# Optimization experiments

Hardware: AMD Instinct MI355X
Metric: run time of the kernel (lower is better)

## Reference

```python
import jax, jax.numpy as jnp
import numpy as np

# Production-scale dims (ENet decoder stage)
B, H, W, C = 8, 128, 128, 64
KH, KW = 2, 2  # kernel_size[1], kernel_size[2]
HOUT, WOUT = H * KH, W * KW


def setup_inputs() -> dict:
    key = jax.random.key(0)
    k1, k2, k3 = jax.random.split(key, 3)
    x = jax.random.normal(k1, (B, H, W, C), dtype=jnp.float32)
    # Build a valid max-pool argmax mask: each pooled cell picks one position
    # inside its KHxKW window; flat index = (h*WOUT + w)*C + c (TF argmax layout).
    dh = jax.random.randint(k2, (B, H, W, C), 0, KH)
    dw = jax.random.randint(k3, (B, H, W, C), 0, KW)
    h = jnp.arange(H)[:, None, None] * KH + dh   # [B,H,W,C]
    w = jnp.arange(W)[None, :, None] * KW + dw   # [B,H,W,C]
    c = jnp.arange(C)                            # [C]
    pool_mask = ((h * WOUT + w) * C + c).astype(jnp.int32)
    return {"input_pool": x, "pool_mask": pool_mask}


def reference(input_pool, pool_mask):
    # Faithful to tf.scatter_nd: decode flat per-batch indices and scatter
    # values into the zero-initialized upsampled output (duplicates add).
    b, h, w, c = input_pool.shape
    out_size = HOUT * WOUT * c
    flat_idx = pool_mask.reshape(b, -1)          # [B, H*W*C] indices into [HOUT*WOUT*C]
    vals = input_pool.reshape(b, -1)
    out = jnp.zeros((b, out_size), dtype=input_pool.dtype)
    out = out.at[jnp.arange(b)[:, None], flat_idx].add(vals)
    return out.reshape(b, HOUT, WOUT, c)
```

## Files before the change

### kernel.cpp

```cpp
#include <hip/hip_runtime.h>


#define Bsz   8
#define Hdim  128
#define Wdim  128
#define Cdim  64
#define HOUT  256
#define WOUT  256

__global__ __launch_bounds__(256) void maxunpool_gather(
    const float4* __restrict__ x,
    const int4*   __restrict__ mask,
    float4*       __restrict__ out)
{
    constexpr int CV = Cdim / 4;
    unsigned int tid = blockIdx.x * blockDim.x + threadIdx.x;

    int c4   = tid & (CV - 1);
    unsigned int r1 = tid >> 4;
    int wo   = r1 & (WOUT - 1);
    unsigned int r2 = r1 >> 8;
    int ho   = r2 & (HOUT - 1);
    int b    = r2 >> 8;

    int h = ho >> 1;
    int w = wo >> 1;

    unsigned int in_vec = ((unsigned int)(b * Hdim + h) * Wdim + w) * CV + c4;

    int4   m = mask[in_vec];
    float4 v = x[in_vec];

    int base = (ho * WOUT + wo) * Cdim + c4 * 4;

    float4 r;
    r.x = (m.x == base + 0) ? v.x : 0.0f;
    r.y = (m.y == base + 1) ? v.y : 0.0f;
    r.z = (m.z == base + 2) ? v.z : 0.0f;
    r.w = (m.w == base + 3) ? v.w : 0.0f;

    out[tid] = r;
}

extern "C" void kernel_launch(void* const* d_in, const int* in_sizes, int n_in,
                              void* d_out, int out_size, void* d_ws, size_t ws_size,
                              hipStream_t stream) {
    const float4* x    = (const float4*)d_in[0];
    const int4*   mask = (const int4*)d_in[1];
    float4*       out  = (float4*)d_out;

    const int n_vec = out_size / 4;
    const int block = 256;
    const int grid  = n_vec / block;

    maxunpool_gather<<<grid, block, 0, stream>>>(x, mask, out);
}
```

Before: 177.9 us.

## Invert unpool to one thread per input, writing 2x2 window with nontemporal ops

Switches from an output-indexed gather, which reloaded each mask and input vector four times, to an input-indexed form. Each thread loads its mask and value once and writes all four output positions of its 2x2 window. Loads and stores use nontemporal builtins to avoid polluting caches with streaming data. The trade-off is four strided stores per thread and a quarter as many threads.

```diff
diff --git a/kernel.cpp b/kernel.cpp
--- a/kernel.cpp
+++ b/kernel.cpp
@@ -1,57 +1,64 @@
 #include <hip/hip_runtime.h>
 
 
-#define Bsz   8
 #define Hdim  128
 #define Wdim  128
 #define Cdim  64
 #define HOUT  256
 #define WOUT  256
+#define CV    (Cdim / 4)
 
-__global__ __launch_bounds__(256) void maxunpool_gather(
-    const float4* __restrict__ x,
-    const int4*   __restrict__ mask,
-    float4*       __restrict__ out)
+typedef float vf4 __attribute__((ext_vector_type(4)));
+typedef int   vi4 __attribute__((ext_vector_type(4)));
+
+__global__ __launch_bounds__(256) void maxunpool_scatter(
+    const vf4* __restrict__ x,
+    const vi4* __restrict__ mask,
+    vf4*       __restrict__ out)
 {
-    constexpr int CV = Cdim / 4;
     unsigned int tid = blockIdx.x * blockDim.x + threadIdx.x;
 
-    int c4   = tid & (CV - 1);
-    unsigned int r1 = tid >> 4;
-    int wo   = r1 & (WOUT - 1);
-    unsigned int r2 = r1 >> 8;
-    int ho   = r2 & (HOUT - 1);
-    int b    = r2 >> 8;
+    int c4 = tid & (CV - 1);
+    unsigned int p = tid >> 4;
+    int w = p & (Wdim - 1);
+    unsigned int q = p >> 7;
+    int h = q & (Hdim - 1);
+    int b = q >> 7;
 
-    int h = ho >> 1;
-    int w = wo >> 1;
+    vi4 m = __builtin_nontemporal_load(&mask[tid]);
+    vf4 v = __builtin_nontemporal_load(&x[tid]);
 
-    unsigned int in_vec = ((unsigned int)(b * Hdim + h) * Wdim + w) * CV + c4;
+    int ho = h << 1;
+    int wo = w << 1;
 
-    int4   m = mask[in_vec];
-    float4 v = x[in_vec];
+    unsigned int o00 = ((unsigned int)(b * HOUT + ho) * WOUT + wo) * CV + c4;
 
-    int base = (ho * WOUT + wo) * Cdim + c4 * 4;
-
-    float4 r;
-    r.x = (m.x == base + 0) ? v.x : 0.0f;
-    r.y = (m.y == base + 1) ? v.y : 0.0f;
-    r.z = (m.z == base + 2) ? v.z : 0.0f;
-    r.w = (m.w == base + 3) ? v.w : 0.0f;
-
-    out[tid] = r;
+    #pragma unroll
+    for (int dh = 0; dh < 2; ++dh) {
+        #pragma unroll
+        for (int dw = 0; dw < 2; ++dw) {
+            int base = ((ho + dh) * WOUT + (wo + dw)) * Cdim + (c4 << 2);
+            vf4 r;
+            r.x = (m.x == base + 0) ? v.x : 0.0f;
+            r.y = (m.y == base + 1) ? v.y : 0.0f;
+            r.z = (m.z == base + 2) ? v.z : 0.0f;
+            r.w = (m.w == base + 3) ? v.w : 0.0f;
+            unsigned int oidx = o00 + (unsigned int)(dh * WOUT + dw) * CV;
+            __builtin_nontemporal_store(r, &out[oidx]);
+        }
+    }
 }
 
 extern "C" void kernel_launch(void* const* d_in, const int* in_sizes, int n_in,
                               void* d_out, int out_size, void* d_ws, size_t ws_size,
                               hipStream_t stream) {
-    const float4* x    = (const float4*)d_in[0];
-    const int4*   mask = (const int4*)d_in[1];
-    float4*       out  = (float4*)d_out;
+    const vf4* x    = (const vf4*)d_in[0];
+    const vi4* mask = (const vi4*)d_in[1];
+    vf4*       out  = (vf4*)d_out;
 
-    const int n_vec = out_size / 4;
+    const int n_vec = in_sizes[0] / 4;
     const int block = 256;
     const int grid  = n_vec / block;
 
-    maxunpool_gather<<<grid, block, 0, stream>>>(x, mask, out);
+    maxunpool_scatter<<<grid, block, 0, stream>>>(x, mask, out);
 }
```

After: 178.3 us. Within noise of the previous version (+0.3%).
